# Kernel tuning notes

Hardware: AMD Instinct MI355X
Metric: run time of the kernel (lower is better)

The kernel has to match this reference:

```python
import jax, jax.numpy as jnp
import numpy as np

N = 50000          # nodes
E = 1_600_000      # edges (avg degree 32)
G = 512            # graphs in batch
IN_DIM = 128
HID = 64


def setup_inputs() -> dict:
    key = jax.random.key(0)
    ks = jax.random.split(key, 9)
    x = jax.random.normal(ks[0], (N, IN_DIM), dtype=jnp.float32)
    edge_index = jax.random.randint(ks[1], (2, E), 0, N, dtype=jnp.int64)
    edge_attr = jax.random.uniform(ks[2], (E,), dtype=jnp.float32)
    batch = jnp.sort(jax.random.randint(ks[3], (N,), 0, G, dtype=jnp.int64))
    W1 = jax.random.normal(ks[4], (IN_DIM, HID), dtype=jnp.float32) / np.sqrt(IN_DIM)
    b1 = jnp.zeros((HID,), dtype=jnp.float32)
    W2 = jax.random.normal(ks[5], (HID, HID), dtype=jnp.float32) / np.sqrt(HID)
    b2 = jnp.zeros((HID,), dtype=jnp.float32)
    Wlin = jax.random.normal(ks[6], (HID, 1), dtype=jnp.float32) / np.sqrt(HID)
    blin = jnp.zeros((1,), dtype=jnp.float32)
    return {"x": x, "edge_index": edge_index, "edge_attr": edge_attr,
            "batch": batch, "W1": W1, "b1": b1, "W2": W2, "b2": b2,
            "Wlin": Wlin, "blin": blin}


def reference(x, edge_index, edge_attr, batch, W1, b1, W2, b2, Wlin, blin):
    n = x.shape[0]
    src, dst = edge_index[0], edge_index[1]
    # GCNConv: add self-loops with weight 1, symmetric normalization
    loop = jnp.arange(n)
    src_f = jnp.concatenate([src, loop])
    dst_f = jnp.concatenate([dst, loop])
    w = jnp.concatenate([edge_attr, jnp.ones((n,), x.dtype)])
    deg = jax.ops.segment_sum(w, dst_f, num_segments=n)
    dis = jnp.where(deg > 0, jax.lax.rsqrt(jnp.maximum(deg, 1e-12)), 0.0)
    norm = dis[src_f] * w * dis[dst_f]  # [E+N]

    def conv(h, W, b):
        hw = h @ W                          # [N, HID]
        msg = norm[:, None] * hw[src_f]     # [E+N, HID]
        return jax.ops.segment_sum(msg, dst_f, num_segments=n) + b

    h = jax.nn.relu(conv(x, W1, b1))
    h = conv(h, W2, b2)
    # global_mean_pool over graph ids
    counts = jax.ops.segment_sum(jnp.ones((n,), h.dtype), batch, num_segments=G)
    pooled = jax.ops.segment_sum(h, batch, num_segments=G) / jnp.maximum(counts, 1.0)[:, None]
    return pooled @ Wlin + blin  # [G, 1]
```

## Files before the change

### kernel.cpp

```cpp
#include <hip/hip_runtime.h>

#define NN 50000
#define NE 1600000
#define NG 512
#define IN_DIM 128
#define HID 64

#define NB 128
#define NBK ((NN + NB - 1) / NB)
#define EBLK 512
#define EPB (NE / EBLK)

typedef unsigned short ushort_t;
typedef unsigned int uint_t;

static __device__ __forceinline__ ushort_t f2bf(float f) {
    uint_t u = __float_as_uint(f);
    u += 0x7FFFu + ((u >> 16) & 1u);
    return (ushort_t)(u >> 16);
}
static __device__ __forceinline__ float bflo(uint_t u) { return __uint_as_float(u << 16); }
static __device__ __forceinline__ float bfhi(uint_t u) { return __uint_as_float(u & 0xFFFF0000u); }

__global__ void cnt_kernel(const int* __restrict__ ei, int* __restrict__ pcnt) {
    __shared__ int h[NBK];
    for (int i = threadIdx.x; i < NBK; i += blockDim.x) h[i] = 0;
    __syncthreads();
    int base = blockIdx.x * EPB;
    for (int e = base + threadIdx.x; e < base + EPB; e += blockDim.x)
        atomicAdd(&h[ei[NE + e] >> 7], 1);
    __syncthreads();
    for (int i = threadIdx.x; i < NBK; i += blockDim.x)
        pcnt[(size_t)i * EBLK + blockIdx.x] = h[i];
}

__global__ void bscan_kernel(int* __restrict__ pcnt, int* __restrict__ tot) {
    __shared__ int s[EBLK];
    int k = blockIdx.x, t = threadIdx.x;
    int v = pcnt[(size_t)k * EBLK + t];
    s[t] = v;
    __syncthreads();
    for (int off = 1; off < EBLK; off <<= 1) {
        int add = (t >= off) ? s[t - off] : 0;
        __syncthreads();
        s[t] += add;
        __syncthreads();
    }
    pcnt[(size_t)k * EBLK + t] = s[t] - v;
    if (t == EBLK - 1) tot[k] = s[t];
}

__global__ void tscan_kernel(const int* __restrict__ tot, int* __restrict__ bbase) {
    __shared__ int s[512];
    int t = threadIdx.x;
    int v = (t < NBK) ? tot[t] : 0;
    s[t] = v;
    __syncthreads();
    for (int off = 1; off < 512; off <<= 1) {
        int add = (t >= off) ? s[t - off] : 0;
        __syncthreads();
        s[t] += add;
        __syncthreads();
    }
    if (t < NBK) bbase[t] = s[t] - v;
    if (t == NBK - 1) bbase[NBK] = s[t];
}

__global__ void scatter_kernel(const int* __restrict__ ei, const float* __restrict__ ea,
                               const int* __restrict__ pcnt, const int* __restrict__ bbase,
                               int2* __restrict__ recs) {
    __shared__ int curs[NBK];
    int b = blockIdx.x;
    for (int i = threadIdx.x; i < NBK; i += blockDim.x)
        curs[i] = bbase[i] + pcnt[(size_t)i * EBLK + b];
    __syncthreads();
    int base = b * EPB;
    for (int e = base + threadIdx.x; e < base + EPB; e += blockDim.x) {
        int dst = ei[NE + e];
        int src = ei[e];
        int k = dst >> 7;
        int pos = atomicAdd(&curs[k], 1);
        recs[pos] = make_int2(((dst & 127) << 17) | src, __float_as_int(ea[e]));
    }
}

__global__ void binfo2_kernel(const int2* __restrict__ recs, const int* __restrict__ bbase,
                              int* __restrict__ indeg, float* __restrict__ dis,
                              int* __restrict__ offs, int2* __restrict__ csr) {
    __shared__ float deg[NB];
    __shared__ int cnt[NB];
    __shared__ int sc[NB];
    __shared__ int curs[NB];
    __shared__ float wdst[NB];
    int k = blockIdx.x;
    int lo = k * NB;
    int nLoc = min(NB, NN - lo);
    int tid = threadIdx.x;
    for (int i = tid; i < nLoc; i += blockDim.x) { deg[i] = 0.f; cnt[i] = 0; }
    __syncthreads();
    int start = bbase[k], end = bbase[k + 1];
    for (int e = start + tid; e < end; e += blockDim.x) {
        int2 r = recs[e];
        int dl = r.x >> 17;
        atomicAdd(&deg[dl], __int_as_float(r.y));
        atomicAdd(&cnt[dl], 1);
    }
    __syncthreads();
    for (int i = tid; i < nLoc; i += blockDim.x) {
        float d = rsqrtf(deg[i] + 1.0f);
        wdst[i] = d;
        dis[lo + i] = d;
        indeg[lo + i] = cnt[i];
    }
    if (tid < NB) sc[tid] = (tid < nLoc) ? cnt[tid] : 0;
    __syncthreads();
    for (int off = 1; off < NB; off <<= 1) {
        int add = (tid < NB && tid >= off) ? sc[tid - off] : 0;
        __syncthreads();
        if (tid < NB) sc[tid] += add;
        __syncthreads();
    }
    if (tid < nLoc) {
        int ex = start + sc[tid] - cnt[tid];
        offs[lo + tid] = ex;
        curs[tid] = ex;
    }
    __syncthreads();
    for (int e = start + tid; e < end; e += blockDim.x) {
        int2 r = recs[e];
        int src = r.x & 0x1FFFF;
        int dl = r.x >> 17;
        float pw = __int_as_float(r.y) * wdst[dl];
        int pos = atomicAdd(&curs[dl], 1);
        csr[pos] = make_int2(src, __float_as_int(pw));
    }
}

template <int K>
__global__ __launch_bounds__(256) void gemm_kernel(const float* __restrict__ X,
                                                   const float* __restrict__ W,
                                                   const float* __restrict__ dis,
                                                   ushort_t* __restrict__ Yb) {
    __shared__ float w_lds[K * HID];
    __shared__ float x_lds[K][65];
    int tid = threadIdx.x;
    int rowbase = blockIdx.x * 64;
    for (int i = tid; i < K * HID; i += 256) w_lds[i] = W[i];
    for (int i = tid; i < 16 * K; i += 256) {
        int row = i / (K / 4);
        int k4 = i % (K / 4);
        int r = rowbase + row;
        float4 v = (r < NN) ? ((const float4*)(X + (size_t)r * K))[k4]
                            : make_float4(0.f, 0.f, 0.f, 0.f);
        x_lds[k4 * 4 + 0][row] = v.x;
        x_lds[k4 * 4 + 1][row] = v.y;
        x_lds[k4 * 4 + 2][row] = v.z;
        x_lds[k4 * 4 + 3][row] = v.w;
    }
    __syncthreads();
    int c0 = (tid & 15) * 4;
    int r0 = (tid >> 4) * 4;
    float acc[4][4] = {};
#pragma unroll 4
    for (int k = 0; k < K; ++k) {
        float x0 = x_lds[k][r0 + 0];
        float x1 = x_lds[k][r0 + 1];
        float x2 = x_lds[k][r0 + 2];
        float x3 = x_lds[k][r0 + 3];
        float4 wv = *(const float4*)&w_lds[k * HID + c0];
        acc[0][0] += x0 * wv.x; acc[0][1] += x0 * wv.y; acc[0][2] += x0 * wv.z; acc[0][3] += x0 * wv.w;
        acc[1][0] += x1 * wv.x; acc[1][1] += x1 * wv.y; acc[1][2] += x1 * wv.z; acc[1][3] += x1 * wv.w;
        acc[2][0] += x2 * wv.x; acc[2][1] += x2 * wv.y; acc[2][2] += x2 * wv.z; acc[2][3] += x2 * wv.w;
        acc[3][0] += x3 * wv.x; acc[3][1] += x3 * wv.y; acc[3][2] += x3 * wv.z; acc[3][3] += x3 * wv.w;
    }
#pragma unroll
    for (int i = 0; i < 4; ++i) {
        int r = rowbase + r0 + i;
        if (r < NN) {
            float dr = dis[r];
            ushort4 o;
            o.x = f2bf(dr * acc[i][0]); o.y = f2bf(dr * acc[i][1]);
            o.z = f2bf(dr * acc[i][2]); o.w = f2bf(dr * acc[i][3]);
            *(ushort4*)&Yb[(size_t)r * HID + c0] = o;
        }
    }
}

template <bool RELU>
__global__ void gather_kernel(const int2* __restrict__ csr,
                              const int* __restrict__ offs,
                              const int* __restrict__ indeg,
                              const float* __restrict__ dis,
                              const ushort_t* __restrict__ HWb,
                              const float* __restrict__ bias,
                              float* __restrict__ OUT) {
    int node = blockIdx.x * 4 + (threadIdx.x >> 6);
    int lane = threadIdx.x & 63;
    if (node >= NN) return;
    int o  = lane >> 3;
    int cl = lane & 7;
    int start = offs[node];
    int n = indeg[node];
    float a0 = 0.f, a1 = 0.f, a2 = 0.f, a3 = 0.f;
    float a4 = 0.f, a5 = 0.f, a6 = 0.f, a7 = 0.f;
    for (int c = 0; c < n; c += 64) {
        int idx = c + lane;
        int2 rec = (idx < n) ? csr[start + idx] : make_int2(0, 0);
        int tmax = min(n - c, 64);
#pragma unroll 2
        for (int t = 0; t * 8 < tmax; ++t) {
            int sl = t * 8 + o;
            int key = __shfl(rec.x, sl, 64);
            float w = __int_as_float(__shfl(rec.y, sl, 64));
            uint4 v = *(const uint4*)(HWb + ((size_t)key << 6) + (cl << 3));
            a0 += w * bflo(v.x); a1 += w * bfhi(v.x);
            a2 += w * bflo(v.y); a3 += w * bfhi(v.y);
            a4 += w * bflo(v.z); a5 += w * bfhi(v.z);
            a6 += w * bflo(v.w); a7 += w * bfhi(v.w);
        }
    }
    a0 += __shfl_xor(a0, 8, 64); a0 += __shfl_xor(a0, 16, 64); a0 += __shfl_xor(a0, 32, 64);
    a1 += __shfl_xor(a1, 8, 64); a1 += __shfl_xor(a1, 16, 64); a1 += __shfl_xor(a1, 32, 64);
    a2 += __shfl_xor(a2, 8, 64); a2 += __shfl_xor(a2, 16, 64); a2 += __shfl_xor(a2, 32, 64);
    a3 += __shfl_xor(a3, 8, 64); a3 += __shfl_xor(a3, 16, 64); a3 += __shfl_xor(a3, 32, 64);
    a4 += __shfl_xor(a4, 8, 64); a4 += __shfl_xor(a4, 16, 64); a4 += __shfl_xor(a4, 32, 64);
    a5 += __shfl_xor(a5, 8, 64); a5 += __shfl_xor(a5, 16, 64); a5 += __shfl_xor(a5, 32, 64);
    a6 += __shfl_xor(a6, 8, 64); a6 += __shfl_xor(a6, 16, 64); a6 += __shfl_xor(a6, 32, 64);
    a7 += __shfl_xor(a7, 8, 64); a7 += __shfl_xor(a7, 16, 64); a7 += __shfl_xor(a7, 32, 64);
    if (o == 0) {
        float d = dis[node];
        uint4 sv = *(const uint4*)(HWb + ((size_t)node << 6) + (cl << 3));
        const float4* bv = (const float4*)(bias + (cl << 3));
        float4 b0 = bv[0], b1 = bv[1];
        float o0 = a0 + d * bflo(sv.x) + b0.x;
        float o1 = a1 + d * bfhi(sv.x) + b0.y;
        float o2 = a2 + d * bflo(sv.y) + b0.z;
        float o3 = a3 + d * bfhi(sv.y) + b0.w;
        float o4 = a4 + d * bflo(sv.z) + b1.x;
        float o5 = a5 + d * bfhi(sv.z) + b1.y;
        float o6 = a6 + d * bflo(sv.w) + b1.z;
        float o7 = a7 + d * bfhi(sv.w) + b1.w;
        if (RELU) {
            o0 = fmaxf(o0, 0.f); o1 = fmaxf(o1, 0.f);
            o2 = fmaxf(o2, 0.f); o3 = fmaxf(o3, 0.f);
            o4 = fmaxf(o4, 0.f); o5 = fmaxf(o5, 0.f);
            o6 = fmaxf(o6, 0.f); o7 = fmaxf(o7, 0.f);
        }
        float* op = &OUT[((size_t)node << 6) + (cl << 3)];
        *(float4*)op       = make_float4(o0, o1, o2, o3);
        *(float4*)(op + 4) = make_float4(o4, o5, o6, o7);
    }
}

__global__ void pool_head_kernel(const float* __restrict__ H,
                                 const int* __restrict__ batch,
                                 const float* __restrict__ Wlin,
                                 const float* __restrict__ blin,
                                 float* __restrict__ out) {
    __shared__ float part[4];
    __shared__ int bnd[2];
    int g = blockIdx.x;
    if (threadIdx.x < 2) {
        int target = g + threadIdx.x;
        int lo = 0, hi = NN;
        while (lo < hi) {
            int mid = (lo + hi) >> 1;
            if (batch[mid] < target) lo = mid + 1; else hi = mid;
        }
        bnd[threadIdx.x] = lo;
    }
    __syncthreads();
    int s = bnd[0], e = bnd[1];
    int lane = threadIdx.x & 63;
    int wv = threadIdx.x >> 6;
    float wl = Wlin[lane];
    float a = 0.f;
    for (int i = s + wv; i < e; i += 4) a += H[(size_t)i * HID + lane];
    float v = a * wl;
    for (int off = 32; off > 0; off >>= 1) v += __shfl_down(v, off, 64);
    if (lane == 0) part[wv] = v;
    __syncthreads();
    if (threadIdx.x == 0) {
        float t = part[0] + part[1] + part[2] + part[3];
        out[g] = t / fmaxf((float)(e - s), 1.0f) + blin[0];
    }
}

extern "C" void kernel_launch(void* const* d_in, const int* in_sizes, int n_in,
                              void* d_out, int out_size, void* d_ws, size_t ws_size,
                              hipStream_t stream) {
    const float* x     = (const float*)d_in[0];
    const int*   ei    = (const int*)d_in[1];
    const float* ea    = (const float*)d_in[2];
    const int*   batch = (const int*)d_in[3];
    const float* W1    = (const float*)d_in[4];
    const float* b1    = (const float*)d_in[5];
    const float* W2    = (const float*)d_in[6];
    const float* b2    = (const float*)d_in[7];
    const float* Wlin  = (const float*)d_in[8];
    const float* blin  = (const float*)d_in[9];
    float*       out   = (float*)d_out;

    char* ws = (char*)d_ws;
    auto alloc = [&](size_t bytes) {
        void* p = (void*)ws;
        ws += (bytes + 255) / 256 * 256;
        return p;
    };
    float*    dis    = (float*)alloc((size_t)NN * 4);
    int*      indeg  = (int*)alloc((size_t)NN * 4);
    int*      offs   = (int*)alloc((size_t)NN * 4);
    int*      pcnt   = (int*)alloc((size_t)NBK * EBLK * 4);
    int*      tot    = (int*)alloc((size_t)NBK * 4);
    int*      bbase  = (int*)alloc((size_t)(NBK + 1) * 4);
    int2*     recs   = (int2*)alloc((size_t)NE * 8);
    int2*     csr    = (int2*)alloc((size_t)NE * 8);
    float*    B      = (float*)alloc((size_t)NN * HID * 4);
    ushort_t* A      = (ushort_t*)recs;

    cnt_kernel<<<EBLK, 256, 0, stream>>>(ei, pcnt);
    bscan_kernel<<<NBK, EBLK, 0, stream>>>(pcnt, tot);
    tscan_kernel<<<1, 512, 0, stream>>>(tot, bbase);
    scatter_kernel<<<EBLK, 256, 0, stream>>>(ei, ea, pcnt, bbase, recs);
    binfo2_kernel<<<NBK, 256, 0, stream>>>(recs, bbase, indeg, dis, offs, csr);

    gemm_kernel<IN_DIM><<<(NN + 63) / 64, 256, 0, stream>>>(x, W1, dis, A);
    gather_kernel<true><<<(NN + 3) / 4, 256, 0, stream>>>(csr, offs, indeg, dis, A, b1, B);

    gemm_kernel<HID><<<(NN + 63) / 64, 256, 0, stream>>>(B, W2, dis, A);
    gather_kernel<false><<<(NN + 3) / 4, 256, 0, stream>>>(csr, offs, indeg, dis, A, b2, B);

    pool_head_kernel<<<NG, 256, 0, stream>>>(B, batch, Wlin, blin, out);
}
```

Before: 174.0 us.

## Fuse second GEMM into first gather and head projection into second gather

The first aggregation kernel now applies bias and ReLU, then multiplies each node row by W2 held in shared memory and writes the bf16 scaled result directly. This removes the fp32 hidden buffer round-trip and the separate second GEMM launch. The second aggregation projects each node onto Wlin and emits one scalar per node, so pooling only sums scalars instead of 64-wide rows. The cost is a 16KB W2 load into LDS per 4-node block (12.5k blocks) plus shuffle-heavy per-node matvec work, which may reduce occupancy.

```diff
diff --git a/kernel.cpp b/kernel.cpp
--- a/kernel.cpp
+++ b/kernel.cpp
@@ -186,14 +186,14 @@
     }
 }
 
-template <bool RELU>
-__global__ void gather_kernel(const int2* __restrict__ csr,
-                              const int* __restrict__ offs,
-                              const int* __restrict__ indeg,
-                              const float* __restrict__ dis,
-                              const ushort_t* __restrict__ HWb,
-                              const float* __restrict__ bias,
-                              float* __restrict__ OUT) {
+__global__ __launch_bounds__(256) void gather1_kernel(
+        const int2* __restrict__ csr, const int* __restrict__ offs,
+        const int* __restrict__ indeg, const float* __restrict__ dis,
+        const ushort_t* __restrict__ A1, const float* __restrict__ b1,
+        const float* __restrict__ W2, ushort_t* __restrict__ A2) {
+    __shared__ float w2_lds[HID * HID];
+    for (int i = threadIdx.x; i < HID * HID; i += 256) w2_lds[i] = W2[i];
+    __syncthreads();
     int node = blockIdx.x * 4 + (threadIdx.x >> 6);
     int lane = threadIdx.x & 63;
     if (node >= NN) return;
@@ -212,7 +212,7 @@
             int sl = t * 8 + o;
             int key = __shfl(rec.x, sl, 64);
             float w = __int_as_float(__shfl(rec.y, sl, 64));
-            uint4 v = *(const uint4*)(HWb + ((size_t)key << 6) + (cl << 3));
+            uint4 v = *(const uint4*)(A1 + ((size_t)key << 6) + (cl << 3));
             a0 += w * bflo(v.x); a1 += w * bfhi(v.x);
             a2 += w * bflo(v.y); a3 += w * bfhi(v.y);
             a4 += w * bflo(v.z); a5 += w * bfhi(v.z);
@@ -227,38 +227,100 @@
     a5 += __shfl_xor(a5, 8, 64); a5 += __shfl_xor(a5, 16, 64); a5 += __shfl_xor(a5, 32, 64);
     a6 += __shfl_xor(a6, 8, 64); a6 += __shfl_xor(a6, 16, 64); a6 += __shfl_xor(a6, 32, 64);
     a7 += __shfl_xor(a7, 8, 64); a7 += __shfl_xor(a7, 16, 64); a7 += __shfl_xor(a7, 32, 64);
-    if (o == 0) {
-        float d = dis[node];
-        uint4 sv = *(const uint4*)(HWb + ((size_t)node << 6) + (cl << 3));
-        const float4* bv = (const float4*)(bias + (cl << 3));
-        float4 b0 = bv[0], b1 = bv[1];
-        float o0 = a0 + d * bflo(sv.x) + b0.x;
-        float o1 = a1 + d * bfhi(sv.x) + b0.y;
-        float o2 = a2 + d * bflo(sv.y) + b0.z;
-        float o3 = a3 + d * bfhi(sv.y) + b0.w;
-        float o4 = a4 + d * bflo(sv.z) + b1.x;
-        float o5 = a5 + d * bfhi(sv.z) + b1.y;
-        float o6 = a6 + d * bflo(sv.w) + b1.z;
-        float o7 = a7 + d * bfhi(sv.w) + b1.w;
-        if (RELU) {
-            o0 = fmaxf(o0, 0.f); o1 = fmaxf(o1, 0.f);
-            o2 = fmaxf(o2, 0.f); o3 = fmaxf(o3, 0.f);
-            o4 = fmaxf(o4, 0.f); o5 = fmaxf(o5, 0.f);
-            o6 = fmaxf(o6, 0.f); o7 = fmaxf(o7, 0.f);
-        }
-        float* op = &OUT[((size_t)node << 6) + (cl << 3)];
-        *(float4*)op       = make_float4(o0, o1, o2, o3);
-        *(float4*)(op + 4) = make_float4(o4, o5, o6, o7);
-    }
-}
-
-__global__ void pool_head_kernel(const float* __restrict__ H,
-                                 const int* __restrict__ batch,
-                                 const float* __restrict__ Wlin,
-                                 const float* __restrict__ blin,
-                                 float* __restrict__ out) {
-    __shared__ float part[4];
+    float d = dis[node];
+    uint4 sv = *(const uint4*)(A1 + ((size_t)node << 6) + (cl << 3));
+    const float4* bv = (const float4*)(b1 + (cl << 3));
+    float4 bA = bv[0], bB = bv[1];
+    float h[8];
+    h[0] = fmaxf(a0 + d * bflo(sv.x) + bA.x, 0.f);
+    h[1] = fmaxf(a1 + d * bfhi(sv.x) + bA.y, 0.f);
+    h[2] = fmaxf(a2 + d * bflo(sv.y) + bA.z, 0.f);
+    h[3] = fmaxf(a3 + d * bfhi(sv.y) + bA.w, 0.f);
+    h[4] = fmaxf(a4 + d * bflo(sv.z) + bB.x, 0.f);
+    h[5] = fmaxf(a5 + d * bfhi(sv.z) + bB.y, 0.f);
+    h[6] = fmaxf(a6 + d * bflo(sv.w) + bB.z, 0.f);
+    h[7] = fmaxf(a7 + d * bfhi(sv.w) + bB.w, 0.f);
+    float acc = 0.f;
+#pragma unroll
+    for (int r = 0; r < 8; ++r) {
+        float hr = h[r];
+#pragma unroll
+        for (int l = 0; l < 8; ++l) {
+            float hv = __shfl(hr, l, 64);
+            acc += hv * w2_lds[(l * 8 + r) * HID + lane];
+        }
+    }
+    A2[((size_t)node << 6) + lane] = f2bf(d * acc);
+}
+
+template <int DUMMY>
+__global__ void gather2_kernel(const int2* __restrict__ csr,
+                               const int* __restrict__ offs,
+                               const int* __restrict__ indeg,
+                               const float* __restrict__ dis,
+                               const ushort_t* __restrict__ A2,
+                               const float* __restrict__ b2,
+                               const float* __restrict__ Wlin,
+                               float* __restrict__ nodeval) {
+    int node = blockIdx.x * 4 + (threadIdx.x >> 6);
+    int lane = threadIdx.x & 63;
+    if (node >= NN) return;
+    int o  = lane >> 3;
+    int cl = lane & 7;
+    int start = offs[node];
+    int n = indeg[node];
+    float a0 = 0.f, a1 = 0.f, a2 = 0.f, a3 = 0.f;
+    float a4 = 0.f, a5 = 0.f, a6 = 0.f, a7 = 0.f;
+    for (int c = 0; c < n; c += 64) {
+        int idx = c + lane;
+        int2 rec = (idx < n) ? csr[start + idx] : make_int2(0, 0);
+        int tmax = min(n - c, 64);
+#pragma unroll 2
+        for (int t = 0; t * 8 < tmax; ++t) {
+            int sl = t * 8 + o;
+            int key = __shfl(rec.x, sl, 64);
+            float w = __int_as_float(__shfl(rec.y, sl, 64));
+            uint4 v = *(const uint4*)(A2 + ((size_t)key << 6) + (cl << 3));
+            a0 += w * bflo(v.x); a1 += w * bfhi(v.x);
+            a2 += w * bflo(v.y); a3 += w * bfhi(v.y);
+            a4 += w * bflo(v.z); a5 += w * bfhi(v.z);
+            a6 += w * bflo(v.w); a7 += w * bfhi(v.w);
+        }
+    }
+    a0 += __shfl_xor(a0, 8, 64); a0 += __shfl_xor(a0, 16, 64); a0 += __shfl_xor(a0, 32, 64);
+    a1 += __shfl_xor(a1, 8, 64); a1 += __shfl_xor(a1, 16, 64); a1 += __shfl_xor(a1, 32, 64);
+    a2 += __shfl_xor(a2, 8, 64); a2 += __shfl_xor(a2, 16, 64); a2 += __shfl_xor(a2, 32, 64);
+    a3 += __shfl_xor(a3, 8, 64); a3 += __shfl_xor(a3, 16, 64); a3 += __shfl_xor(a3, 32, 64);
+    a4 += __shfl_xor(a4, 8, 64); a4 += __shfl_xor(a4, 16, 64); a4 += __shfl_xor(a4, 32, 64);
+    a5 += __shfl_xor(a5, 8, 64); a5 += __shfl_xor(a5, 16, 64); a5 += __shfl_xor(a5, 32, 64);
+    a6 += __shfl_xor(a6, 8, 64); a6 += __shfl_xor(a6, 16, 64); a6 += __shfl_xor(a6, 32, 64);
+    a7 += __shfl_xor(a7, 8, 64); a7 += __shfl_xor(a7, 16, 64); a7 += __shfl_xor(a7, 32, 64);
+    float d = dis[node];
+    uint4 sv = *(const uint4*)(A2 + ((size_t)node << 6) + (cl << 3));
+    const float4* bv = (const float4*)(b2 + (cl << 3));
+    float4 bA = bv[0], bB = bv[1];
+    const float4* wv = (const float4*)(Wlin + (cl << 3));
+    float4 wA = wv[0], wB = wv[1];
+    float dot = (a0 + d * bflo(sv.x) + bA.x) * wA.x
+              + (a1 + d * bfhi(sv.x) + bA.y) * wA.y
+              + (a2 + d * bflo(sv.y) + bA.z) * wA.z
+              + (a3 + d * bfhi(sv.y) + bA.w) * wA.w
+              + (a4 + d * bflo(sv.z) + bB.x) * wB.x
+              + (a5 + d * bfhi(sv.z) + bB.y) * wB.y
+              + (a6 + d * bflo(sv.w) + bB.z) * wB.z
+              + (a7 + d * bfhi(sv.w) + bB.w) * wB.w;
+    dot += __shfl_xor(dot, 1, 64);
+    dot += __shfl_xor(dot, 2, 64);
+    dot += __shfl_xor(dot, 4, 64);
+    if (lane == 0) nodeval[node] = dot;
+}
+
+__global__ void pool_final_kernel(const float* __restrict__ nodeval,
+                                  const int* __restrict__ batch,
+                                  const float* __restrict__ blin,
+                                  float* __restrict__ out) {
     __shared__ int bnd[2];
+    __shared__ float red[4];
     int g = blockIdx.x;
     if (threadIdx.x < 2) {
         int target = g + threadIdx.x;
@@ -271,17 +333,15 @@
     }
     __syncthreads();
     int s = bnd[0], e = bnd[1];
+    float a = 0.f;
+    for (int i = s + threadIdx.x; i < e; i += 256) a += nodeval[i];
+    for (int off = 32; off > 0; off >>= 1) a += __shfl_down(a, off, 64);
     int lane = threadIdx.x & 63;
     int wv = threadIdx.x >> 6;
-    float wl = Wlin[lane];
-    float a = 0.f;
-    for (int i = s + wv; i < e; i += 4) a += H[(size_t)i * HID + lane];
-    float v = a * wl;
-    for (int off = 32; off > 0; off >>= 1) v += __shfl_down(v, off, 64);
-    if (lane == 0) part[wv] = v;
+    if (lane == 0) red[wv] = a;
     __syncthreads();
     if (threadIdx.x == 0) {
-        float t = part[0] + part[1] + part[2] + part[3];
+        float t = red[0] + red[1] + red[2] + red[3];
         out[g] = t / fmaxf((float)(e - s), 1.0f) + blin[0];
     }
 }
@@ -307,16 +367,17 @@
         ws += (bytes + 255) / 256 * 256;
         return p;
     };
-    float*    dis    = (float*)alloc((size_t)NN * 4);
-    int*      indeg  = (int*)alloc((size_t)NN * 4);
-    int*      offs   = (int*)alloc((size_t)NN * 4);
-    int*      pcnt   = (int*)alloc((size_t)NBK * EBLK * 4);
-    int*      tot    = (int*)alloc((size_t)NBK * 4);
-    int*      bbase  = (int*)alloc((size_t)(NBK + 1) * 4);
-    int2*     recs   = (int2*)alloc((size_t)NE * 8);
-    int2*     csr    = (int2*)alloc((size_t)NE * 8);
-    float*    B      = (float*)alloc((size_t)NN * HID * 4);
-    ushort_t* A      = (ushort_t*)recs;
+    float*    dis     = (float*)alloc((size_t)NN * 4);
+    int*      indeg   = (int*)alloc((size_t)NN * 4);
+    int*      offs    = (int*)alloc((size_t)NN * 4);
+    int*      pcnt    = (int*)alloc((size_t)NBK * EBLK * 4);
+    int*      tot     = (int*)alloc((size_t)NBK * 4);
+    int*      bbase   = (int*)alloc((size_t)(NBK + 1) * 4);
+    int2*     recs    = (int2*)alloc((size_t)NE * 8);
+    int2*     csr     = (int2*)alloc((size_t)NE * 8);
+    ushort_t* A2      = (ushort_t*)alloc((size_t)NN * HID * 2);
+    float*    nodeval = (float*)alloc((size_t)NN * 4);
+    ushort_t* A1      = (ushort_t*)recs;
 
     cnt_kernel<<<EBLK, 256, 0, stream>>>(ei, pcnt);
     bscan_kernel<<<NBK, EBLK, 0, stream>>>(pcnt, tot);
@@ -324,11 +385,12 @@
     scatter_kernel<<<EBLK, 256, 0, stream>>>(ei, ea, pcnt, bbase, recs);
     binfo2_kernel<<<NBK, 256, 0, stream>>>(recs, bbase, indeg, dis, offs, csr);
 
-    gemm_kernel<IN_DIM><<<(NN + 63) / 64, 256, 0, stream>>>(x, W1, dis, A);
-    gather_kernel<true><<<(NN + 3) / 4, 256, 0, stream>>>(csr, offs, indeg, dis, A, b1, B);
-
-    gemm_kernel<HID><<<(NN + 63) / 64, 256, 0, stream>>>(B, W2, dis, A);
-    gather_kernel<false><<<(NN + 3) / 4, 256, 0, stream>>>(csr, offs, indeg, dis, A, b2, B);
-
-    pool_head_kernel<<<NG, 256, 0, stream>>>(B, batch, Wlin, blin, out);
-}
+    gemm_kernel<IN_DIM><<<(NN + 63) / 64, 256, 0, stream>>>(x, W1, dis, A1);
+
+    gather1_kernel<<<(NN + 3) / 4, 256, 0, stream>>>(csr, offs, indeg, dis, A1, b1, W2, A2);
+
+    gather2_kernel<0><<<(NN + 3) / 4, 256, 0, stream>>>(csr, offs, indeg, dis, A2, b2,
+                                                        Wlin, nodeval);
+
+    pool_final_kernel<<<NG, 256, 0, stream>>>(nodeval, batch, blin, out);
+}
```

Result: slower. 194.1 us (+11.5%).
